# Performance work log

Hardware: AMD Instinct MI355X
Metric: run time of the kernel (lower is better)

Reference implementation:

```python
import jax, jax.numpy as jnp
import numpy as np

BATCH = 4096          # batch_size from init
TEMP = 0.1            # temperature
EPS = 1e-8            # torch CosineSimilarity eps
N = 2 * BATCH


def _neg_flat_idx(bs):
    """Static flat indices of the negative entries of the (N,N) sim matrix:
    everything except the main diagonal and the +-bs diagonals (positives)."""
    n = 2 * bs
    mask = np.ones((n, n), dtype=bool)
    np.fill_diagonal(mask, False)
    r = np.arange(bs)
    mask[r, bs + r] = False
    mask[bs + r, r] = False
    return np.nonzero(mask.reshape(-1))[0]


NEG_IDX = jnp.asarray(_neg_flat_idx(BATCH))  # (N*(N-2),)


def setup_inputs() -> dict:
    key = jax.random.key(0)
    k1, k2 = jax.random.split(key)
    msg = jax.random.normal(k1, (N, 512), dtype=jnp.float32)
    img = jax.random.normal(k2, (N, 512), dtype=jnp.float32)
    return {"msg": msg, "img": img}


def reference(msg, img):
    # cosine similarity via normalized GEMM (norms clamped at eps, per torch)
    mn = msg / jnp.maximum(jnp.linalg.norm(msg, axis=1, keepdims=True), EPS)
    im = img / jnp.maximum(jnp.linalg.norm(img, axis=1, keepdims=True), EPS)
    sim = jnp.matmul(mn, im.T) / TEMP                      # (N, N)

    sim_i_j = jnp.diagonal(sim, offset=BATCH)              # (BATCH,)
    sim_j_i = jnp.diagonal(sim, offset=-BATCH)             # (BATCH,)
    positives = jnp.concatenate([sim_i_j, sim_j_i])[:, None]   # (N, 1)
    negatives = sim.reshape(-1)[NEG_IDX].reshape(N, N - 2)     # (N, N-2)

    logits = jnp.concatenate([positives, negatives], axis=1)   # (N, N-1)
    logp = jax.nn.log_softmax(logits, axis=1)
    # labels are all zero; CrossEntropyLoss(reduction='sum') / N
    loss = -jnp.sum(logp[:, 0]) / N
    acc = jnp.mean((jnp.argmax(logits, axis=1) == 0).astype(jnp.float32))
    return loss, acc
```

## Files before the change

### kernel.cpp

```cpp
#include <hip/hip_runtime.h>
#include <hip/hip_bf16.h>


#define NROWS 8192
#define BATCHD 4096
#define DIM 512
#define BM 256
#define BN 256
#define BK 64
#define NT (DIM / BK)
#define SHIFT 10.0f

typedef short bf16x8 __attribute__((ext_vector_type(8)));
typedef float f32x4 __attribute__((ext_vector_type(4)));

#define GLDS(g, l)                                                             \
    __builtin_amdgcn_global_load_lds(                                          \
        (const __attribute__((address_space(1))) void*)(g),                    \
        (__attribute__((address_space(3))) void*)(l), 16, 0, 0)

__device__ __forceinline__ unsigned f2u_ord(float f) {
    unsigned u = __float_as_uint(f);
    return (u & 0x80000000u) ? ~u : (u | 0x80000000u);
}
__device__ __forceinline__ float u2f_ord(unsigned e) {
    return (e & 0x80000000u) ? __uint_as_float(e & 0x7fffffffu) : __uint_as_float(~e);
}
__device__ __forceinline__ short f2bf(float f) {
    unsigned u = __float_as_uint(f);
    return (short)((u + 0x7fffu + ((u >> 16) & 1u)) >> 16);
}

__global__ __launch_bounds__(64) void normalize_bf16_both(const float* __restrict__ msg,
                                                          const float* __restrict__ img,
                                                          short* __restrict__ mnb,
                                                          short* __restrict__ imb,
                                                          float* __restrict__ rowsum,
                                                          unsigned* __restrict__ rowmax,
                                                          float* __restrict__ accum) {
    if (blockIdx.x < 128) {
        const int i = blockIdx.x * 64 + threadIdx.x;
        rowsum[i] = 0.f;
        rowmax[i] = 0u;
        if (i < 2) accum[i] = 0.f;
    }
    int row = blockIdx.x;
    const float* in;
    short* out;
    float scale;
    if (row < NROWS) { in = msg; out = mnb; scale = 10.0f; }
    else { row -= NROWS; in = img; out = imb; scale = 1.0f; }
    const int lane = threadIdx.x;
    const float* src = in + (size_t)row * DIM + lane * 8;
    float4 v0 = *(const float4*)(src);
    float4 v1 = *(const float4*)(src + 4);
    float ss = v0.x*v0.x + v0.y*v0.y + v0.z*v0.z + v0.w*v0.w
             + v1.x*v1.x + v1.y*v1.y + v1.z*v1.z + v1.w*v1.w;
    #pragma unroll
    for (int off = 1; off < 64; off <<= 1) ss += __shfl_xor(ss, off);
    const float inv = scale / fmaxf(sqrtf(ss), 1e-8f);
    float vv[8] = {v0.x, v0.y, v0.z, v0.w, v1.x, v1.y, v1.z, v1.w};
    bf16x8 o;
    #pragma unroll
    for (int j = 0; j < 8; ++j) o[j] = f2bf(vv[j] * inv);
    *(bf16x8*)(out + (size_t)row * DIM + lane * 8) = o;
}

__global__ __launch_bounds__(512, 2) void simloss_mfma(const short* __restrict__ A,
                                                       const short* __restrict__ B,
                                                       float* __restrict__ rowsum,
                                                       unsigned* __restrict__ rowmax,
                                                       float* __restrict__ rowpos) {
    __shared__ short As[2][2][BM * 32];
    __shared__ short Bs[2][2][BN * 32];

    const int tid = threadIdx.x;
    const int lane = tid & 63;
    const int g = lane >> 4;
    const int r16 = lane & 15;
    const int wid = tid >> 6;
    const int wr = wid >> 2;
    const int wc = wid & 3;

    const int bid = blockIdx.x;
    const int k = bid & 7;
    const int l = bid >> 3;
    const int by = k * 4 + (l & 3);
    const int bx = l >> 2;
    const int rowBase = by * BM;
    const int colBase = bx * BN;

    const int s0 = tid, s1 = 512 + tid;
    const int row0 = s0 >> 2, row1 = s1 >> 2;
    const int c0 = (s0 & 3) ^ ((row0 >> 1) & 3);
    const int c1 = (s1 & 3) ^ ((row1 >> 1) & 3);
    const short* gA0 = A + (size_t)(rowBase + row0) * DIM + c0 * 8;
    const short* gA1 = A + (size_t)(rowBase + row1) * DIM + c1 * 8;
    const short* gB0 = B + (size_t)(colBase + row0) * DIM + c0 * 8;
    const short* gB1 = B + (size_t)(colBase + row1) * DIM + c1 * 8;

#define STAGE_A(b, kh, koff)                                        \
    do {                                                            \
        GLDS(gA0 + (koff) + (kh) * 32, &As[b][kh][tid * 8]);        \
        GLDS(gA1 + (koff) + (kh) * 32, &As[b][kh][4096 + tid * 8]); \
    } while (0)
#define STAGE_B(b, kh, koff)                                        \
    do {                                                            \
        GLDS(gB0 + (koff) + (kh) * 32, &Bs[b][kh][tid * 8]);        \
        GLDS(gB1 + (koff) + (kh) * 32, &Bs[b][kh][4096 + tid * 8]); \
    } while (0)

    const int swz = (r16 >> 1) & 3;
    const int aBase = (wr * 128 + r16) * 32 + ((g ^ swz) * 8);
    const int bBase = (wc * 64 + r16) * 32 + ((g ^ swz) * 8);

    f32x4 acc[8][4] = {};
    bf16x8 af[4], bfr[4];

#define DS_A(b, ks, mh)                                                        \
    do {                                                                       \
        _Pragma("unroll") for (int m = 0; m < 4; ++m)                          \
            af[m] = *(const bf16x8*)&As[b][ks][aBase + (mh) * 2048 + m * 512]; \
    } while (0)
#define DS_B(b, ks)                                                            \
    do {                                                                       \
        _Pragma("unroll") for (int n = 0; n < 4; ++n)                          \
            bfr[n] = *(const bf16x8*)&Bs[b][ks][bBase + n * 512];              \
    } while (0)
#define MFMA16(mh)                                                             \
    do {                                                                       \
        __builtin_amdgcn_s_setprio(1);                                         \
        _Pragma("unroll") for (int m = 0; m < 4; ++m)                          \
            _Pragma("unroll") for (int n = 0; n < 4; ++n)                      \
                acc[(mh) * 4 + m][n] = __builtin_amdgcn_mfma_f32_16x16x32_bf16(\
                    af[m], bfr[n], acc[(mh) * 4 + m][n], 0, 0, 0);             \
        __builtin_amdgcn_s_setprio(0);                                         \
    } while (0)
#define VMCNT(n) asm volatile("s_waitcnt vmcnt(" #n ")" ::: "memory")
#define BAR() __builtin_amdgcn_s_barrier()

    STAGE_A(0, 0, 0);
    STAGE_B(0, 0, 0);
    STAGE_A(0, 1, 0);
    STAGE_B(0, 1, 0);
    VMCNT(4);
    BAR();

    for (int t = 0; t < NT; ++t) {
        const int b = t & 1;
        const int koff = (t + 1) * BK;
        const bool st = (t + 1 < NT);
        DS_A(b, 0, 0);
        DS_B(b, 0);
        if (st) { STAGE_A(b ^ 1, 0, koff); STAGE_B(b ^ 1, 0, koff); }
        BAR();
        MFMA16(0);
        BAR();
        DS_A(b, 0, 1);
        if (st) { STAGE_A(b ^ 1, 1, koff); STAGE_B(b ^ 1, 1, koff); }
        BAR();
        MFMA16(1);
        if (st) VMCNT(8);
        else    VMCNT(0);
        BAR();
        DS_A(b, 1, 0);
        DS_B(b, 1);
        BAR();
        MFMA16(0);
        BAR();
        DS_A(b, 1, 1);
        BAR();
        MFMA16(1);
        if (st) VMCNT(4);
        BAR();
    }

    float* ssum = (float*)&As[0][0][0];
    float* smx = ssum + 1024;
    const int baseRowW = rowBase + wr * 128 + g * 4;
    const int baseColW = colBase + wc * 64 + r16;
    #pragma unroll
    for (int m = 0; m < 8; ++m) {
        #pragma unroll
        for (int reg = 0; reg < 4; ++reg) {
            const int i = baseRowW + m * 16 + reg;
            const int partner = i ^ BATCHD;
            float sum = 0.f, mx = -1e30f;
            #pragma unroll
            for (int n = 0; n < 4; ++n) {
                const int j = baseColW + n * 16;
                const float s = acc[m][n][reg];
                const bool isDiag = (j == i);
                const bool isPos = (j == partner);
                float e = __expf(s - SHIFT);
                if (isDiag) e = 0.f;
                sum += e;
                if (!isDiag && !isPos) mx = fmaxf(mx, s);
                if (isPos) rowpos[i] = s;
            }
            #pragma unroll
            for (int off = 1; off < 16; off <<= 1) {
                sum += __shfl_xor(sum, off);
                mx = fmaxf(mx, __shfl_xor(mx, off));
            }
            if (r16 == 0) {
                const int rloc = wr * 128 + m * 16 + g * 4 + reg;
                ssum[rloc * 4 + wc] = sum;
                smx[rloc * 4 + wc] = mx;
            }
        }
    }
    __syncthreads();
    if (tid < 256) {
        const float s = ssum[tid * 4 + 0] + ssum[tid * 4 + 1] +
                        ssum[tid * 4 + 2] + ssum[tid * 4 + 3];
        const float mx = fmaxf(fmaxf(smx[tid * 4 + 0], smx[tid * 4 + 1]),
                               fmaxf(smx[tid * 4 + 2], smx[tid * 4 + 3]));
        const int i = rowBase + tid;
        atomicAdd(&rowsum[i], s);
        atomicMax(&rowmax[i], f2u_ord(mx));
    }
#undef STAGE_A
#undef STAGE_B
#undef DS_A
#undef DS_B
#undef MFMA16
#undef VMCNT
#undef BAR
}

__global__ __launch_bounds__(256) void finalize_partial(const float* __restrict__ rowsum,
                                                        const unsigned* __restrict__ rowmax,
                                                        const float* __restrict__ rowpos,
                                                        float* __restrict__ accum) {
    const int tid = threadIdx.x;
    const int i = blockIdx.x * 256 + tid;
    const float lse = SHIFT + logf(rowsum[i]);
    const float pos = rowpos[i];
    float lossAcc = lse - pos;
    float hitAcc = (pos >= u2f_ord(rowmax[i])) ? 1.f : 0.f;
    __shared__ float sl[256], sa[256];
    sl[tid] = lossAcc; sa[tid] = hitAcc;
    __syncthreads();
    for (int s = 128; s > 0; s >>= 1) {
        if (tid < s) { sl[tid] += sl[tid + s]; sa[tid] += sa[tid + s]; }
        __syncthreads();
    }
    if (tid == 0) {
        atomicAdd(&accum[0], sl[0]);
        atomicAdd(&accum[1], sa[0]);
    }
}

__global__ void finalize_write(const float* __restrict__ accum, float* __restrict__ out) {
    if (threadIdx.x == 0) {
        out[0] = accum[0] / (float)NROWS;
        out[1] = accum[1] / (float)NROWS;
    }
}

extern "C" void kernel_launch(void* const* d_in, const int* in_sizes, int n_in,
                              void* d_out, int out_size, void* d_ws, size_t ws_size,
                              hipStream_t stream) {
    const float* msg = (const float*)d_in[0];
    const float* img = (const float*)d_in[1];
    float* out = (float*)d_out;

    char* ws = (char*)d_ws;
    const size_t matBytes = (size_t)NROWS * DIM * sizeof(short);
    short* mnb = (short*)ws;
    short* imb = (short*)(ws + matBytes);
    float* rowsum = (float*)(ws + 2 * matBytes);
    unsigned* rowmax = (unsigned*)(ws + 2 * matBytes + NROWS * sizeof(float));
    float* rowpos = (float*)(ws + 2 * matBytes + 2 * NROWS * sizeof(float));
    float* accum = (float*)(ws + 2 * matBytes + 3 * NROWS * sizeof(float));

    normalize_bf16_both<<<2 * NROWS, 64, 0, stream>>>(msg, img, mnb, imb,
                                                      rowsum, rowmax, accum);

    simloss_mfma<<<(NROWS / BM) * (NROWS / BN), 512, 0, stream>>>(mnb, imb, rowsum,
                                                                  rowmax, rowpos);

    finalize_partial<<<NROWS / 256, 256, 0, stream>>>(rowsum, rowmax, rowpos, accum);
    finalize_write<<<1, 64, 0, stream>>>(accum, out);
}
```

Baseline: 117.4 us.

## Double-buffer MFMA fragments in registers to overlap LDS reads with MFMA

Replaces the single af/bfr fragment set with two register sets so that LDS reads for the next MFMA group are issued while the current group computes. The number of barriers per K-tile drops from eight to four, and the loop is fully unrolled. The first fragments of the next tile are prefetched before the tile's last MFMA group. This hides LDS latency and cuts barrier stalls, at the cost of more VGPRs and a more delicate ordering between global-to-LDS staging and reads.

```diff
diff --git a/kernel.cpp b/kernel.cpp
--- a/kernel.cpp
+++ b/kernel.cpp
@@ -115,25 +115,25 @@
     const int bBase = (wc * 64 + r16) * 32 + ((g ^ swz) * 8);
 
     f32x4 acc[8][4] = {};
-    bf16x8 af[4], bfr[4];
-
-#define DS_A(b, ks, mh)                                                        \
-    do {                                                                       \
-        _Pragma("unroll") for (int m = 0; m < 4; ++m)                          \
-            af[m] = *(const bf16x8*)&As[b][ks][aBase + (mh) * 2048 + m * 512]; \
-    } while (0)
-#define DS_B(b, ks)                                                            \
-    do {                                                                       \
-        _Pragma("unroll") for (int n = 0; n < 4; ++n)                          \
-            bfr[n] = *(const bf16x8*)&Bs[b][ks][bBase + n * 512];              \
-    } while (0)
-#define MFMA16(mh)                                                             \
+    bf16x8 aR0[4], aR1[4], bR0[4], bR1[4];
+
+#define READ_A(b, ks, mh, dst)                                                  \
+    do {                                                                        \
+        _Pragma("unroll") for (int m = 0; m < 4; ++m)                           \
+            dst[m] = *(const bf16x8*)&As[b][ks][aBase + (mh) * 2048 + m * 512]; \
+    } while (0)
+#define READ_B(b, ks, dst)                                                      \
+    do {                                                                        \
+        _Pragma("unroll") for (int n = 0; n < 4; ++n)                           \
+            dst[n] = *(const bf16x8*)&Bs[b][ks][bBase + n * 512];               \
+    } while (0)
+#define MFMA16(mh, Af, Bf)                                                     \
     do {                                                                       \
         __builtin_amdgcn_s_setprio(1);                                         \
         _Pragma("unroll") for (int m = 0; m < 4; ++m)                          \
             _Pragma("unroll") for (int n = 0; n < 4; ++n)                      \
                 acc[(mh) * 4 + m][n] = __builtin_amdgcn_mfma_f32_16x16x32_bf16(\
-                    af[m], bfr[n], acc[(mh) * 4 + m][n], 0, 0, 0);             \
+                    Af[m], Bf[n], acc[(mh) * 4 + m][n], 0, 0, 0);              \
         __builtin_amdgcn_s_setprio(0);                                         \
     } while (0)
 #define VMCNT(n) asm volatile("s_waitcnt vmcnt(" #n ")" ::: "memory")
@@ -145,36 +145,37 @@
     STAGE_B(0, 1, 0);
     VMCNT(4);
     BAR();
-
+    READ_A(0, 0, 0, aR0);
+    READ_B(0, 0, bR0);
+
+    #pragma unroll
     for (int t = 0; t < NT; ++t) {
         const int b = t & 1;
         const int koff = (t + 1) * BK;
-        const bool st = (t + 1 < NT);
-        DS_A(b, 0, 0);
-        DS_B(b, 0);
-        if (st) { STAGE_A(b ^ 1, 0, koff); STAGE_B(b ^ 1, 0, koff); }
-        BAR();
-        MFMA16(0);
-        BAR();
-        DS_A(b, 0, 1);
-        if (st) { STAGE_A(b ^ 1, 1, koff); STAGE_B(b ^ 1, 1, koff); }
-        BAR();
-        MFMA16(1);
-        if (st) VMCNT(8);
-        else    VMCNT(0);
-        BAR();
-        DS_A(b, 1, 0);
-        DS_B(b, 1);
-        BAR();
-        MFMA16(0);
-        BAR();
-        DS_A(b, 1, 1);
-        BAR();
-        MFMA16(1);
-        if (st) VMCNT(4);
-        BAR();
-    }
-
+        BAR();
+        if (t < NT - 1) { STAGE_A(b ^ 1, 0, koff); STAGE_B(b ^ 1, 0, koff); }
+        READ_A(b, 0, 1, aR1);
+        MFMA16(0, aR0, bR0);
+        if (t < NT - 1) VMCNT(4);
+        else            VMCNT(0);
+        BAR();
+        if (t < NT - 1) { STAGE_A(b ^ 1, 1, koff); STAGE_B(b ^ 1, 1, koff); }
+        READ_A(b, 1, 0, aR0);
+        READ_B(b, 1, bR1);
+        MFMA16(1, aR1, bR0);
+        BAR();
+        READ_A(b, 1, 1, aR1);
+        MFMA16(0, aR0, bR1);
+        if (t < NT - 1) VMCNT(4);
+        BAR();
+        if (t < NT - 1) {
+            READ_A(b ^ 1, 0, 0, aR0);
+            READ_B(b ^ 1, 0, bR0);
+        }
+        MFMA16(1, aR1, bR1);
+    }
+
+    __syncthreads();
     float* ssum = (float*)&As[0][0][0];
     float* smx = ssum + 1024;
     const int baseRowW = rowBase + wr * 128 + g * 4;
@@ -222,8 +223,8 @@
     }
 #undef STAGE_A
 #undef STAGE_B
-#undef DS_A
-#undef DS_B
+#undef READ_A
+#undef READ_B
 #undef MFMA16
 #undef VMCNT
 #undef BAR
```

Measured after the change: 110.9 us. 5.5% less time.
